# Kernel optimization log

Hardware: AMD Instinct MI355X
Metric: run time of the kernel (lower is better)

Reference implementation:

```python
import jax, jax.numpy as jnp
import numpy as np

N, L, S, H, D = 2, 4096, 4096, 8, 64


def setup_inputs() -> dict:
    key = jax.random.key(0)
    kq, kk, kv = jax.random.split(key, 3)
    queries = jax.random.normal(kq, (N, L, H, D), dtype=jnp.float32)
    keys = jax.random.normal(kk, (N, S, H, D), dtype=jnp.float32)
    values = jax.random.normal(kv, (N, S, H, D), dtype=jnp.float32)
    return {"queries": queries, "keys": keys, "values": values}


def reference(queries, keys, values):
    # Full (non-fused) scaled dot-product attention, LoFTR FullAttention.
    # QK: [N, L, S, H]
    softmax_temp = 1.0 / jnp.sqrt(jnp.asarray(queries.shape[3], queries.dtype))
    QK = jnp.einsum('nlhd,nshd->nlsh', queries, keys)
    A = jax.nn.softmax(softmax_temp * QK, axis=2)  # softmax over S
    out = jnp.einsum('nlsh,nshd->nlhd', A, values)  # [N, L, H, D]
    return out
```

## Files before the change

### kernel.cpp

```cpp
#include <hip/hip_runtime.h>
#include <hip/hip_bf16.h>

typedef float  f32x4  __attribute__((ext_vector_type(4)));
typedef float  f32x16 __attribute__((ext_vector_type(16)));
typedef short  short8 __attribute__((ext_vector_type(8)));
typedef int    i32x2  __attribute__((ext_vector_type(2)));
typedef unsigned int uint4v __attribute__((ext_vector_type(4)));

#define N_  2
#define L_  4096
#define S_  4096
#define H_  8
#define D_  64
#define HD_ 512
#define KVB 64
#define QB  128
#define NTL 32

__device__ __forceinline__ unsigned short f2bf(float f) {
  unsigned int u = __builtin_bit_cast(unsigned int, f);
  u += 0x7fffu + ((u >> 16) & 1u);
  return (unsigned short)(u >> 16);
}
__device__ __forceinline__ unsigned short bf16c(float f) {
  return __builtin_bit_cast(unsigned short, __float2bfloat16(f));
}
__device__ __forceinline__ unsigned int pk2(float lo, float hi) {
  unsigned int r;
  asm("v_cvt_pk_bf16_f32 %0, %1, %2" : "=v"(r) : "v"(lo), "v"(hi));
  return r;
}
__device__ __forceinline__ f32x16 zero16() {
  f32x16 v;
  #pragma unroll
  for (int i = 0; i < 16; ++i) v[i] = 0.f;
  return v;
}
__device__ __forceinline__ float tsum16(const f32x16& v) {
  float a0 = v[0] + v[1],   a1 = v[2] + v[3];
  float a2 = v[4] + v[5],   a3 = v[6] + v[7];
  float a4 = v[8] + v[9],   a5 = v[10] + v[11];
  float a6 = v[12] + v[13], a7 = v[14] + v[15];
  float b0 = a0 + a1, b1 = a2 + a3, b2 = a4 + a5, b3 = a6 + a7;
  return (b0 + b1) + (b2 + b3);
}

__global__ __launch_bounds__(256, 8)
void prepack(const float* __restrict__ Kg, const float* __restrict__ Vg,
             unsigned short* __restrict__ Kw, unsigned short* __restrict__ Vw) {
  const int b = blockIdx.x;
  const int tid = threadIdx.x;
  const int isV = (b >= 1024);
  const int tb = isV ? b - 1024 : b;
  const int nh = tb >> 6, t = tb & 63;
  const int n = nh >> 3, h = nh & 7;

  if (!isV) {
    const int sl = tid >> 2, d0 = (tid & 3) << 4;
    const float* src = Kg + ((size_t)(n * S_ + t * 64 + sl) * H_ + h) * D_ + d0;
    f32x4 x0 = *(const f32x4*)(src);
    f32x4 x1 = *(const f32x4*)(src + 4);
    f32x4 x2 = *(const f32x4*)(src + 8);
    f32x4 x3 = *(const f32x4*)(src + 12);
    short8 t0, t1;
    t0[0] = (short)f2bf(x0[0]); t0[1] = (short)f2bf(x0[1]);
    t0[2] = (short)f2bf(x0[2]); t0[3] = (short)f2bf(x0[3]);
    t0[4] = (short)f2bf(x1[0]); t0[5] = (short)f2bf(x1[1]);
    t0[6] = (short)f2bf(x1[2]); t0[7] = (short)f2bf(x1[3]);
    t1[0] = (short)f2bf(x2[0]); t1[1] = (short)f2bf(x2[1]);
    t1[2] = (short)f2bf(x2[2]); t1[3] = (short)f2bf(x2[3]);
    t1[4] = (short)f2bf(x3[0]); t1[5] = (short)f2bf(x3[1]);
    t1[6] = (short)f2bf(x3[2]); t1[7] = (short)f2bf(x3[3]);
    unsigned short* dst = Kw + (size_t)tb * 4096;
    const int b0 = d0 >> 3;
    *(short8*)&dst[(b0)     * 512 + sl * 8] = t0;
    *(short8*)&dst[(b0 + 1) * 512 + sl * 8] = t1;
  } else {
    const int d = tid & 63, sb2 = tid >> 6;
    #pragma unroll
    for (int c = 0; c < 2; ++c) {
      const int sblk = sb2 * 2 + c;
      const float* src = Vg + ((size_t)(n * S_ + t * 64 + sblk * 8) * H_ + h) * D_ + d;
      short8 o;
      #pragma unroll
      for (int j = 0; j < 8; ++j) o[j] = (short)f2bf(src[(size_t)j * HD_]);
      *(short8*)&Vw[(size_t)tb * 4096 + sblk * 512 + d * 8] = o;
    }
  }
}

template<int W1, int Wa, int Wb, int DOK, int DOV>
__device__ __forceinline__ void tile_body(
    int t, const char* kbase, const char* vbase,
    const short8 qf[4], short8 kf0[4], short8 kf1[4], short8 vf[8],
    f32x16& acc0, f32x16& acc1, float& lsum)
{
  asm volatile("s_waitcnt vmcnt(%0)" :: "n"(W1) : "memory");
  __builtin_amdgcn_sched_barrier(0);
  f32x16 s0a = zero16();
  __builtin_amdgcn_s_setprio(1);
  #pragma unroll
  for (int kc = 0; kc < 4; ++kc)
    s0a = __builtin_amdgcn_mfma_f32_32x32x16_bf16(kf0[kc], qf[kc], s0a, 0, 0, 0);
  __builtin_amdgcn_s_setprio(0);

  if (DOK) {
    const char* kp = kbase + (size_t)(t + 1) * 8192;
    #pragma unroll
    for (int kc = 0; kc < 4; ++kc)
      kf0[kc] = *(const short8*)(kp + kc * 2048);
  }

  #pragma unroll
  for (int r = 0; r < 16; ++r) s0a[r] = __builtin_amdgcn_exp2f(s0a[r]);
  lsum += tsum16(s0a);

  asm volatile("s_waitcnt vmcnt(%0)" :: "n"(Wa) : "memory");
  __builtin_amdgcn_sched_barrier(0);
  #pragma unroll
  for (int sc = 0; sc < 2; ++sc) {
    const unsigned int c0 = pk2(s0a[8 * sc + 0], s0a[8 * sc + 1]);
    const unsigned int c1 = pk2(s0a[8 * sc + 2], s0a[8 * sc + 3]);
    const unsigned int c2 = pk2(s0a[8 * sc + 4], s0a[8 * sc + 5]);
    const unsigned int c3 = pk2(s0a[8 * sc + 6], s0a[8 * sc + 7]);
    i32x2 r0 = __builtin_amdgcn_permlane32_swap((int)c0, (int)c2, false, false);
    i32x2 r1 = __builtin_amdgcn_permlane32_swap((int)c1, (int)c3, false, false);
    uint4v w = { (unsigned)r0[0], (unsigned)r1[0], (unsigned)r0[1], (unsigned)r1[1] };
    const short8 pa = __builtin_bit_cast(short8, w);
    __builtin_amdgcn_s_setprio(1);
    acc0 = __builtin_amdgcn_mfma_f32_32x32x16_bf16(pa, vf[sc * 2 + 0], acc0, 0, 0, 0);
    acc1 = __builtin_amdgcn_mfma_f32_32x32x16_bf16(pa, vf[sc * 2 + 1], acc1, 0, 0, 0);
    __builtin_amdgcn_s_setprio(0);
  }

  f32x16 s1a = zero16();
  __builtin_amdgcn_s_setprio(1);
  #pragma unroll
  for (int kc = 0; kc < 4; ++kc)
    s1a = __builtin_amdgcn_mfma_f32_32x32x16_bf16(kf1[kc], qf[kc], s1a, 0, 0, 0);
  __builtin_amdgcn_s_setprio(0);

  if (DOK) {
    const char* kp = kbase + (size_t)(t + 1) * 8192 + 512;
    #pragma unroll
    for (int kc = 0; kc < 4; ++kc)
      kf1[kc] = *(const short8*)(kp + kc * 2048);
  }

  #pragma unroll
  for (int r = 0; r < 16; ++r) s1a[r] = __builtin_amdgcn_exp2f(s1a[r]);
  lsum += tsum16(s1a);

  asm volatile("s_waitcnt vmcnt(%0)" :: "n"(Wb) : "memory");
  __builtin_amdgcn_sched_barrier(0);
  #pragma unroll
  for (int sc = 0; sc < 2; ++sc) {
    const unsigned int c0 = pk2(s1a[8 * sc + 0], s1a[8 * sc + 1]);
    const unsigned int c1 = pk2(s1a[8 * sc + 2], s1a[8 * sc + 3]);
    const unsigned int c2 = pk2(s1a[8 * sc + 4], s1a[8 * sc + 5]);
    const unsigned int c3 = pk2(s1a[8 * sc + 6], s1a[8 * sc + 7]);
    i32x2 r0 = __builtin_amdgcn_permlane32_swap((int)c0, (int)c2, false, false);
    i32x2 r1 = __builtin_amdgcn_permlane32_swap((int)c1, (int)c3, false, false);
    uint4v w = { (unsigned)r0[0], (unsigned)r1[0], (unsigned)r0[1], (unsigned)r1[1] };
    const short8 pa = __builtin_bit_cast(short8, w);
    __builtin_amdgcn_s_setprio(1);
    acc0 = __builtin_amdgcn_mfma_f32_32x32x16_bf16(pa, vf[4 + sc * 2 + 0], acc0, 0, 0, 0);
    acc1 = __builtin_amdgcn_mfma_f32_32x32x16_bf16(pa, vf[4 + sc * 2 + 1], acc1, 0, 0, 0);
    __builtin_amdgcn_s_setprio(0);
  }

  if (DOV) {
    const char* vp = vbase + (size_t)(t + 1) * 8192;
    #pragma unroll
    for (int q8 = 0; q8 < 8; ++q8)
      vf[q8] = *(const short8*)(vp + (q8 >> 1) * 2048 + (q8 & 1) * 512);
  }
}

__global__ __launch_bounds__(512, 2)
void attn_fa6(const float* __restrict__ Qg,
              const unsigned short* __restrict__ Kw,
              const unsigned short* __restrict__ Vw,
              float* __restrict__ Og) {
  __shared__ __align__(16) float Comb[4][2048];
  __shared__ float CombL[4][32];

  const int tid = threadIdx.x;
  const int wv  = tid >> 6;
  const int qw  = wv & 3;
  const int sh  = wv >> 2;
  const int ln  = tid & 63;
  const int hi  = ln >> 5;
  const int c32 = ln & 31;

  const int bid = blockIdx.x;
  const int swz = (bid & 7) * 64 + (bid >> 3);
  const int qt  = swz & 31;
  const int nh  = swz >> 5;
  const int h = nh & 7, n = nh >> 3;
  const int qbase = qt * QB;

  const float qs = 0.125f * 1.44269504088896340736f;
  const int qrow = qbase + (qw << 5) + c32;
  const float* qp = Qg + (size_t)(n * L_ + qrow) * HD_ + h * D_ + (hi << 3);
  short8 qf[4];
  #pragma unroll
  for (int kc = 0; kc < 4; ++kc) {
    const float* p = qp + (kc << 4);
    f32x4 a = *(const f32x4*)(p);
    f32x4 b = *(const f32x4*)(p + 4);
    short8 f;
    f[0] = (short)bf16c(a[0] * qs); f[1] = (short)bf16c(a[1] * qs);
    f[2] = (short)bf16c(a[2] * qs); f[3] = (short)bf16c(a[3] * qs);
    f[4] = (short)bf16c(b[0] * qs); f[5] = (short)bf16c(b[1] * qs);
    f[6] = (short)bf16c(b[2] * qs); f[7] = (short)bf16c(b[3] * qs);
    qf[kc] = f;
  }
  asm volatile("s_waitcnt vmcnt(0)" ::: "memory");

  f32x16 acc0 = zero16(), acc1 = zero16();
  float lsum = 0.f;

  const char* kbase = (const char*)(Kw + (size_t)nh * 64 * 4096)
                      + (size_t)sh * NTL * 8192 + (hi << 10) + (c32 << 4);
  const char* vbase = (const char*)(Vw + (size_t)nh * 64 * 4096)
                      + (size_t)sh * NTL * 8192 + (hi << 10) + (c32 << 4);

  short8 kf0[4], kf1[4], vf[8];

  #pragma unroll
  for (int kc = 0; kc < 4; ++kc) {
    kf0[kc] = *(const short8*)(kbase + kc * 2048);
    kf1[kc] = *(const short8*)(kbase + kc * 2048 + 512);
  }
  #pragma unroll
  for (int q8 = 0; q8 < 8; ++q8)
    vf[q8] = *(const short8*)(vbase + (q8 >> 1) * 2048 + (q8 & 1) * 512);

  for (int t = 0; t < NTL - 1; ++t)
    tile_body<8, 8, 8, 1, 1>(t, kbase, vbase, qf, kf0, kf1, vf, acc0, acc1, lsum);
  tile_body<8, 4, 0, 0, 0>(NTL - 1, kbase, vbase, qf, kf0, kf1, vf, acc0, acc1, lsum);

  const float full = lsum + __shfl_xor(lsum, 32);
  float* C = &Comb[qw][0];

  if (sh == 1) {
    #pragma unroll
    for (int r = 0; r < 16; ++r) {
      const int q = (r & 3) + 8 * (r >> 2) + 4 * hi;
      C[q * 64 + c32]      = acc0[r];
      C[q * 64 + 32 + c32] = acc1[r];
    }
    if (hi == 0) CombL[qw][c32] = full;
  }
  __syncthreads();
  if (sh == 0) {
    const float ltot = full + CombL[qw][c32];
    #pragma unroll
    for (int r = 0; r < 16; ++r) {
      const int q = (r & 3) + 8 * (r >> 2) + 4 * hi;
      const float l = __shfl(ltot, q);
      const float inv = 1.f / l;
      const int row = qbase + (qw << 5) + q;
      float* op = Og + (size_t)(n * L_ + row) * HD_ + h * D_ + c32;
      op[0]  = (acc0[r] + C[q * 64 + c32]) * inv;
      op[32] = (acc1[r] + C[q * 64 + 32 + c32]) * inv;
    }
  }
}

extern "C" void kernel_launch(void* const* d_in, const int* in_sizes, int n_in,
                              void* d_out, int out_size, void* d_ws, size_t ws_size,
                              hipStream_t stream) {
  (void)in_sizes; (void)n_in; (void)out_size; (void)ws_size;
  const float* Q = (const float*)d_in[0];
  const float* K = (const float*)d_in[1];
  const float* V = (const float*)d_in[2];
  float* O = (float*)d_out;

  unsigned short* Kw = (unsigned short*)d_ws;
  unsigned short* Vw = Kw + 4194304;
  hipLaunchKernelGGL(prepack, dim3(2048), dim3(256), 0, stream, K, V, Kw, Vw);
  hipLaunchKernelGGL(attn_fa6, dim3(512), dim3(512), 0, stream, Q, Kw, Vw, O);
}
```

Before: 100.4 us.

## Give each wave two query sub-tiles and split KV within tiles

Each wave now holds two 32-row query fragments and reuses every K and V fragment it loads for both, which halves the per-wave global-load traffic per unit of MFMA work. Blocks drop from 8 to 4 waves. The two KV halves are now split by interleaving 32-key halves inside each 64-key tile instead of by contiguous halves of the sequence. This adds register pressure from four accumulators and two Q fragment sets, and leaves fewer waves per CU to hide latency. The final normalisation now uses division instead of a multiply by a reciprocal.

```diff
diff --git a/kernel.cpp b/kernel.cpp
--- a/kernel.cpp
+++ b/kernel.cpp
@@ -15,7 +15,7 @@
 #define HD_ 512
 #define KVB 64
 #define QB  128
-#define NTL 32
+#define NT  64
 
 __device__ __forceinline__ unsigned short f2bf(float f) {
   unsigned int u = __builtin_bit_cast(unsigned int, f);
@@ -89,106 +89,102 @@
   }
 }
 
-template<int W1, int Wa, int Wb, int DOK, int DOV>
-__device__ __forceinline__ void tile_body(
-    int t, const char* kbase, const char* vbase,
-    const short8 qf[4], short8 kf0[4], short8 kf1[4], short8 vf[8],
-    f32x16& acc0, f32x16& acc1, float& lsum)
-{
-  asm volatile("s_waitcnt vmcnt(%0)" :: "n"(W1) : "memory");
-  __builtin_amdgcn_sched_barrier(0);
-  f32x16 s0a = zero16();
-  __builtin_amdgcn_s_setprio(1);
-  #pragma unroll
-  for (int kc = 0; kc < 4; ++kc)
-    s0a = __builtin_amdgcn_mfma_f32_32x32x16_bf16(kf0[kc], qf[kc], s0a, 0, 0, 0);
-  __builtin_amdgcn_s_setprio(0);
-
-  if (DOK) {
-    const char* kp = kbase + (size_t)(t + 1) * 8192;
-    #pragma unroll
-    for (int kc = 0; kc < 4; ++kc)
-      kf0[kc] = *(const short8*)(kp + kc * 2048);
-  }
-
-  #pragma unroll
-  for (int r = 0; r < 16; ++r) s0a[r] = __builtin_amdgcn_exp2f(s0a[r]);
-  lsum += tsum16(s0a);
-
-  asm volatile("s_waitcnt vmcnt(%0)" :: "n"(Wa) : "memory");
-  __builtin_amdgcn_sched_barrier(0);
-  #pragma unroll
-  for (int sc = 0; sc < 2; ++sc) {
-    const unsigned int c0 = pk2(s0a[8 * sc + 0], s0a[8 * sc + 1]);
-    const unsigned int c1 = pk2(s0a[8 * sc + 2], s0a[8 * sc + 3]);
-    const unsigned int c2 = pk2(s0a[8 * sc + 4], s0a[8 * sc + 5]);
-    const unsigned int c3 = pk2(s0a[8 * sc + 6], s0a[8 * sc + 7]);
+__device__ __forceinline__ void mk_pa(const f32x16& s, short8& pa0, short8& pa1) {
+  {
+    const unsigned int c0 = pk2(s[0], s[1]);
+    const unsigned int c1 = pk2(s[2], s[3]);
+    const unsigned int c2 = pk2(s[4], s[5]);
+    const unsigned int c3 = pk2(s[6], s[7]);
     i32x2 r0 = __builtin_amdgcn_permlane32_swap((int)c0, (int)c2, false, false);
     i32x2 r1 = __builtin_amdgcn_permlane32_swap((int)c1, (int)c3, false, false);
     uint4v w = { (unsigned)r0[0], (unsigned)r1[0], (unsigned)r0[1], (unsigned)r1[1] };
-    const short8 pa = __builtin_bit_cast(short8, w);
-    __builtin_amdgcn_s_setprio(1);
-    acc0 = __builtin_amdgcn_mfma_f32_32x32x16_bf16(pa, vf[sc * 2 + 0], acc0, 0, 0, 0);
-    acc1 = __builtin_amdgcn_mfma_f32_32x32x16_bf16(pa, vf[sc * 2 + 1], acc1, 0, 0, 0);
-    __builtin_amdgcn_s_setprio(0);
-  }
-
-  f32x16 s1a = zero16();
-  __builtin_amdgcn_s_setprio(1);
-  #pragma unroll
-  for (int kc = 0; kc < 4; ++kc)
-    s1a = __builtin_amdgcn_mfma_f32_32x32x16_bf16(kf1[kc], qf[kc], s1a, 0, 0, 0);
-  __builtin_amdgcn_s_setprio(0);
-
-  if (DOK) {
-    const char* kp = kbase + (size_t)(t + 1) * 8192 + 512;
-    #pragma unroll
-    for (int kc = 0; kc < 4; ++kc)
-      kf1[kc] = *(const short8*)(kp + kc * 2048);
-  }
-
-  #pragma unroll
-  for (int r = 0; r < 16; ++r) s1a[r] = __builtin_amdgcn_exp2f(s1a[r]);
-  lsum += tsum16(s1a);
-
-  asm volatile("s_waitcnt vmcnt(%0)" :: "n"(Wb) : "memory");
-  __builtin_amdgcn_sched_barrier(0);
-  #pragma unroll
-  for (int sc = 0; sc < 2; ++sc) {
-    const unsigned int c0 = pk2(s1a[8 * sc + 0], s1a[8 * sc + 1]);
-    const unsigned int c1 = pk2(s1a[8 * sc + 2], s1a[8 * sc + 3]);
-    const unsigned int c2 = pk2(s1a[8 * sc + 4], s1a[8 * sc + 5]);
-    const unsigned int c3 = pk2(s1a[8 * sc + 6], s1a[8 * sc + 7]);
+    pa0 = __builtin_bit_cast(short8, w);
+  }
+  {
+    const unsigned int c0 = pk2(s[8],  s[9]);
+    const unsigned int c1 = pk2(s[10], s[11]);
+    const unsigned int c2 = pk2(s[12], s[13]);
+    const unsigned int c3 = pk2(s[14], s[15]);
     i32x2 r0 = __builtin_amdgcn_permlane32_swap((int)c0, (int)c2, false, false);
     i32x2 r1 = __builtin_amdgcn_permlane32_swap((int)c1, (int)c3, false, false);
     uint4v w = { (unsigned)r0[0], (unsigned)r1[0], (unsigned)r0[1], (unsigned)r1[1] };
-    const short8 pa = __builtin_bit_cast(short8, w);
-    __builtin_amdgcn_s_setprio(1);
-    acc0 = __builtin_amdgcn_mfma_f32_32x32x16_bf16(pa, vf[4 + sc * 2 + 0], acc0, 0, 0, 0);
-    acc1 = __builtin_amdgcn_mfma_f32_32x32x16_bf16(pa, vf[4 + sc * 2 + 1], acc1, 0, 0, 0);
-    __builtin_amdgcn_s_setprio(0);
-  }
+    pa1 = __builtin_bit_cast(short8, w);
+  }
+}
+
+template<int WK, int WV, int DOK, int DOV>
+__device__ __forceinline__ void tile_body(
+    int t, const char* kbase, const char* vbase,
+    const short8 qfA[4], const short8 qfB[4], short8 kf[4], short8 vf[4],
+    f32x16& accA0, f32x16& accA1, f32x16& accB0, f32x16& accB1,
+    float& lsumA, float& lsumB)
+{
+  asm volatile("s_waitcnt vmcnt(%0)" :: "n"(WK) : "memory");
+  __builtin_amdgcn_sched_barrier(0);
+
+  f32x16 sA = zero16(), sB = zero16();
+  __builtin_amdgcn_s_setprio(1);
+  #pragma unroll
+  for (int kc = 0; kc < 4; ++kc)
+    sA = __builtin_amdgcn_mfma_f32_32x32x16_bf16(kf[kc], qfA[kc], sA, 0, 0, 0);
+  #pragma unroll
+  for (int kc = 0; kc < 4; ++kc)
+    sB = __builtin_amdgcn_mfma_f32_32x32x16_bf16(kf[kc], qfB[kc], sB, 0, 0, 0);
+  __builtin_amdgcn_s_setprio(0);
+
+  if (DOK) {
+    const char* kp = kbase + (size_t)(t + 1) * 8192;
+    #pragma unroll
+    for (int kc = 0; kc < 4; ++kc)
+      kf[kc] = *(const short8*)(kp + kc * 2048);
+  }
+
+  #pragma unroll
+  for (int r = 0; r < 16; ++r) sA[r] = __builtin_amdgcn_exp2f(sA[r]);
+  lsumA += tsum16(sA);
+  #pragma unroll
+  for (int r = 0; r < 16; ++r) sB[r] = __builtin_amdgcn_exp2f(sB[r]);
+  lsumB += tsum16(sB);
+
+  asm volatile("s_waitcnt vmcnt(%0)" :: "n"(WV) : "memory");
+  __builtin_amdgcn_sched_barrier(0);
+
+  short8 paA0, paA1, paB0, paB1;
+  mk_pa(sA, paA0, paA1);
+  __builtin_amdgcn_s_setprio(1);
+  accA0 = __builtin_amdgcn_mfma_f32_32x32x16_bf16(paA0, vf[0], accA0, 0, 0, 0);
+  accA1 = __builtin_amdgcn_mfma_f32_32x32x16_bf16(paA0, vf[1], accA1, 0, 0, 0);
+  accA0 = __builtin_amdgcn_mfma_f32_32x32x16_bf16(paA1, vf[2], accA0, 0, 0, 0);
+  accA1 = __builtin_amdgcn_mfma_f32_32x32x16_bf16(paA1, vf[3], accA1, 0, 0, 0);
+  __builtin_amdgcn_s_setprio(0);
+  mk_pa(sB, paB0, paB1);
+  __builtin_amdgcn_s_setprio(1);
+  accB0 = __builtin_amdgcn_mfma_f32_32x32x16_bf16(paB0, vf[0], accB0, 0, 0, 0);
+  accB1 = __builtin_amdgcn_mfma_f32_32x32x16_bf16(paB0, vf[1], accB1, 0, 0, 0);
+  accB0 = __builtin_amdgcn_mfma_f32_32x32x16_bf16(paB1, vf[2], accB0, 0, 0, 0);
+  accB1 = __builtin_amdgcn_mfma_f32_32x32x16_bf16(paB1, vf[3], accB1, 0, 0, 0);
+  __builtin_amdgcn_s_setprio(0);
 
   if (DOV) {
     const char* vp = vbase + (size_t)(t + 1) * 8192;
     #pragma unroll
-    for (int q8 = 0; q8 < 8; ++q8)
-      vf[q8] = *(const short8*)(vp + (q8 >> 1) * 2048 + (q8 & 1) * 512);
-  }
-}
-
-__global__ __launch_bounds__(512, 2)
-void attn_fa6(const float* __restrict__ Qg,
+    for (int q4 = 0; q4 < 4; ++q4)
+      vf[q4] = *(const short8*)(vp + (q4 >> 1) * 2048 + (q4 & 1) * 512);
+  }
+}
+
+__global__ __launch_bounds__(256, 2)
+void attn_fa7(const float* __restrict__ Qg,
               const unsigned short* __restrict__ Kw,
               const unsigned short* __restrict__ Vw,
               float* __restrict__ Og) {
-  __shared__ __align__(16) float Comb[4][2048];
-  __shared__ float CombL[4][32];
+  __shared__ __align__(16) float Comb[2][4096];
+  __shared__ float CombL[2][64];
 
   const int tid = threadIdx.x;
   const int wv  = tid >> 6;
-  const int qw  = wv & 3;
-  const int sh  = wv >> 2;
+  const int qw  = wv & 1;
+  const int sh  = wv >> 1;
   const int ln  = tid & 63;
   const int hi  = ln >> 5;
   const int c32 = ln & 31;
@@ -198,73 +194,83 @@
   const int qt  = swz & 31;
   const int nh  = swz >> 5;
   const int h = nh & 7, n = nh >> 3;
-  const int qbase = qt * QB;
+  const int qbase = qt * QB + qw * 64;
 
   const float qs = 0.125f * 1.44269504088896340736f;
-  const int qrow = qbase + (qw << 5) + c32;
-  const float* qp = Qg + (size_t)(n * L_ + qrow) * HD_ + h * D_ + (hi << 3);
-  short8 qf[4];
-  #pragma unroll
-  for (int kc = 0; kc < 4; ++kc) {
-    const float* p = qp + (kc << 4);
-    f32x4 a = *(const f32x4*)(p);
-    f32x4 b = *(const f32x4*)(p + 4);
-    short8 f;
-    f[0] = (short)bf16c(a[0] * qs); f[1] = (short)bf16c(a[1] * qs);
-    f[2] = (short)bf16c(a[2] * qs); f[3] = (short)bf16c(a[3] * qs);
-    f[4] = (short)bf16c(b[0] * qs); f[5] = (short)bf16c(b[1] * qs);
-    f[6] = (short)bf16c(b[2] * qs); f[7] = (short)bf16c(b[3] * qs);
-    qf[kc] = f;
+  short8 qfA[4], qfB[4];
+  #pragma unroll
+  for (int b = 0; b < 2; ++b) {
+    const int qrow = qbase + b * 32 + c32;
+    const float* qp = Qg + (size_t)(n * L_ + qrow) * HD_ + h * D_ + (hi << 3);
+    #pragma unroll
+    for (int kc = 0; kc < 4; ++kc) {
+      const float* p = qp + (kc << 4);
+      f32x4 a = *(const f32x4*)(p);
+      f32x4 bx = *(const f32x4*)(p + 4);
+      short8 f;
+      f[0] = (short)bf16c(a[0] * qs);  f[1] = (short)bf16c(a[1] * qs);
+      f[2] = (short)bf16c(a[2] * qs);  f[3] = (short)bf16c(a[3] * qs);
+      f[4] = (short)bf16c(bx[0] * qs); f[5] = (short)bf16c(bx[1] * qs);
+      f[6] = (short)bf16c(bx[2] * qs); f[7] = (short)bf16c(bx[3] * qs);
+      if (b == 0) qfA[kc] = f; else qfB[kc] = f;
+    }
   }
   asm volatile("s_waitcnt vmcnt(0)" ::: "memory");
 
-  f32x16 acc0 = zero16(), acc1 = zero16();
-  float lsum = 0.f;
+  f32x16 accA0 = zero16(), accA1 = zero16(), accB0 = zero16(), accB1 = zero16();
+  float lsumA = 0.f, lsumB = 0.f;
 
   const char* kbase = (const char*)(Kw + (size_t)nh * 64 * 4096)
-                      + (size_t)sh * NTL * 8192 + (hi << 10) + (c32 << 4);
+                      + (hi << 10) + (sh << 9) + (c32 << 4);
   const char* vbase = (const char*)(Vw + (size_t)nh * 64 * 4096)
-                      + (size_t)sh * NTL * 8192 + (hi << 10) + (c32 << 4);
-
-  short8 kf0[4], kf1[4], vf[8];
-
-  #pragma unroll
-  for (int kc = 0; kc < 4; ++kc) {
-    kf0[kc] = *(const short8*)(kbase + kc * 2048);
-    kf1[kc] = *(const short8*)(kbase + kc * 2048 + 512);
-  }
-  #pragma unroll
-  for (int q8 = 0; q8 < 8; ++q8)
-    vf[q8] = *(const short8*)(vbase + (q8 >> 1) * 2048 + (q8 & 1) * 512);
-
-  for (int t = 0; t < NTL - 1; ++t)
-    tile_body<8, 8, 8, 1, 1>(t, kbase, vbase, qf, kf0, kf1, vf, acc0, acc1, lsum);
-  tile_body<8, 4, 0, 0, 0>(NTL - 1, kbase, vbase, qf, kf0, kf1, vf, acc0, acc1, lsum);
-
-  const float full = lsum + __shfl_xor(lsum, 32);
+                      + (sh << 12) + (hi << 10) + (c32 << 4);
+
+  short8 kf[4], vf[4];
+  #pragma unroll
+  for (int kc = 0; kc < 4; ++kc)
+    kf[kc] = *(const short8*)(kbase + kc * 2048);
+  #pragma unroll
+  for (int q4 = 0; q4 < 4; ++q4)
+    vf[q4] = *(const short8*)(vbase + (q4 >> 1) * 2048 + (q4 & 1) * 512);
+
+  for (int t = 0; t < NT - 1; ++t)
+    tile_body<4, 4, 1, 1>(t, kbase, vbase, qfA, qfB, kf, vf,
+                          accA0, accA1, accB0, accB1, lsumA, lsumB);
+  tile_body<4, 0, 0, 0>(NT - 1, kbase, vbase, qfA, qfB, kf, vf,
+                        accA0, accA1, accB0, accB1, lsumA, lsumB);
+
+  const float fullA = lsumA + __shfl_xor(lsumA, 32);
+  const float fullB = lsumB + __shfl_xor(lsumB, 32);
   float* C = &Comb[qw][0];
 
   if (sh == 1) {
     #pragma unroll
     for (int r = 0; r < 16; ++r) {
       const int q = (r & 3) + 8 * (r >> 2) + 4 * hi;
-      C[q * 64 + c32]      = acc0[r];
-      C[q * 64 + 32 + c32] = acc1[r];
-    }
-    if (hi == 0) CombL[qw][c32] = full;
+      C[q * 64 + c32]             = accA0[r];
+      C[q * 64 + 32 + c32]        = accA1[r];
+      C[(32 + q) * 64 + c32]      = accB0[r];
+      C[(32 + q) * 64 + 32 + c32] = accB1[r];
+    }
+    if (hi == 0) { CombL[qw][c32] = fullA; CombL[qw][32 + c32] = fullB; }
   }
   __syncthreads();
   if (sh == 0) {
-    const float ltot = full + CombL[qw][c32];
+    const float ltotA = fullA + CombL[qw][c32];
+    const float ltotB = fullB + CombL[qw][32 + c32];
     #pragma unroll
     for (int r = 0; r < 16; ++r) {
       const int q = (r & 3) + 8 * (r >> 2) + 4 * hi;
-      const float l = __shfl(ltot, q);
-      const float inv = 1.f / l;
-      const int row = qbase + (qw << 5) + q;
-      float* op = Og + (size_t)(n * L_ + row) * HD_ + h * D_ + c32;
-      op[0]  = (acc0[r] + C[q * 64 + c32]) * inv;
-      op[32] = (acc1[r] + C[q * 64 + 32 + c32]) * inv;
+      const float lA = __shfl(ltotA, q);
+      const float lB = __shfl(ltotB, q);
+      const int rowA = qbase + q;
+      const int rowB = qbase + 32 + q;
+      float* opA = Og + (size_t)(n * L_ + rowA) * HD_ + h * D_ + c32;
+      float* opB = Og + (size_t)(n * L_ + rowB) * HD_ + h * D_ + c32;
+      opA[0]  = (accA0[r] + C[q * 64 + c32])             / lA;
+      opA[32] = (accA1[r] + C[q * 64 + 32 + c32])        / lA;
+      opB[0]  = (accB0[r] + C[(32 + q) * 64 + c32])      / lB;
+      opB[32] = (accB1[r] + C[(32 + q) * 64 + 32 + c32]) / lB;
     }
   }
 }
@@ -281,5 +287,5 @@
   unsigned short* Kw = (unsigned short*)d_ws;
   unsigned short* Vw = Kw + 4194304;
   hipLaunchKernelGGL(prepack, dim3(2048), dim3(256), 0, stream, K, V, Kw, Vw);
-  hipLaunchKernelGGL(attn_fa6, dim3(512), dim3(512), 0, stream, Q, Kw, Vw, O);
-}
+  hipLaunchKernelGGL(attn_fa7, dim3(512), dim3(256), 0, stream, Q, Kw, Vw, O);
+}
```

Result: faster. 93.46 us (-6.9%).
